# Kernel tuning notes

Hardware: AMD Instinct MI355X
Metric: run time of the kernel (lower is better)

Reference implementation:

```python
import jax, jax.numpy as jnp
import numpy as np

GAMMA = 0.01      # rbf gamma (init kwarg)
C = 10            # n_classes (len(nv))
NV = 500          # support vectors per class (equal segments)
# all (i, j) class pairs with i < j, in the original nested-loop order
PAIRS = np.array([(i, j) for i in range(C) for j in range(i + 1, C)], dtype=np.int32)
I_IDX = jnp.asarray(PAIRS[:, 0])  # [45]
J_IDX = jnp.asarray(PAIRS[:, 1])  # [45]


def setup_inputs() -> dict:
    key = jax.random.key(0)
    k1, k2, k3, k4 = jax.random.split(key, 4)
    x = jax.random.normal(k1, (8192, 256), dtype=jnp.float32)
    sv = jax.random.normal(k2, (5000, 256), dtype=jnp.float32)
    a = jax.random.normal(k3, (C - 1, 5000), dtype=jnp.float32) * 0.1  # dual coefs
    b = jax.random.normal(k4, (45,), dtype=jnp.float32) * 0.1          # intercepts per pair
    return {"x": x, "sv": sv, "a": a, "b": b}


def reference(x, sv, a, b):
    # RBF kernel matrix: k[n, s] = exp(-gamma * ||x_n - sv_s||^2)
    x_norm = jnp.sum(x * x, axis=1)[:, None]            # [N, 1]
    sv_norm = jnp.sum(sv * sv, axis=1)[None, :]         # [1, SV]
    k = jnp.exp(-GAMMA * (x_norm + sv_norm) + 2.0 * GAMMA * (x @ sv.T))  # [N, SV]

    N = x.shape[0]
    kr = k.reshape(N, C, NV)           # per-class SV segments
    ar = a.reshape(C - 1, C, NV)       # dual coef rows, segmented the same way
    # T[n, r, c] = sum_m a[r, segment c, m] * k[n, segment c, m]
    # (fuses every inner Python loop of the original into one contraction)
    T = jnp.einsum('ncm,rcm->nrc', kr, ar)              # [N, C-1, C]

    # decision for pair (i, j): a[i, seg j] . k_seg_j + a[j-1, seg i] . k_seg_i + b
    c = T[:, I_IDX, J_IDX] + T[:, J_IDX - 1, I_IDX] + b[None, :]  # [N, 45]

    # pairwise voting: winner i if c > 0 else j; class id = mode of votes
    votes = jnp.where(c > 0, I_IDX[None, :], J_IDX[None, :])      # [N, 45] int32
    counts = jnp.sum(jax.nn.one_hot(votes, C, dtype=jnp.float32), axis=1)  # [N, C]
    # argmax picks the smallest class index on ties, matching torch.mode
    class_ids = jnp.argmax(counts, axis=1).astype(jnp.int32)
    return (class_ids, class_ids)
```

## Files before the change

kernel.cpp:

```cpp
#include <hip/hip_runtime.h>
#include <hip/hip_fp16.h>
#include <cmath>


#define GAMMA 0.01f
constexpr int N  = 8192;
constexpr int D  = 256;
constexpr int S  = 5000;
constexpr int C  = 10;
constexpr int NV = 500;
constexpr int R  = 9;
constexpr int SPAD = 5120;

typedef _Float16 f16x8 __attribute__((ext_vector_type(8)));
typedef _Float16 f16x4 __attribute__((ext_vector_type(4)));
typedef float    f32x4 __attribute__((ext_vector_type(4)));

__device__ __forceinline__ void gload16(const void* g, void* l) {
    __builtin_amdgcn_global_load_lds(
        (const __attribute__((address_space(1))) void*)g,
        (__attribute__((address_space(3))) void*)l, 16, 0, 0);
}

__global__ __launch_bounds__(256) void prep_kernel(const float* __restrict__ x,
                                                   const float* __restrict__ sv,
                                                   _Float16* __restrict__ xh,
                                                   _Float16* __restrict__ xl,
                                                   _Float16* __restrict__ sh,
                                                   _Float16* __restrict__ sl,
                                                   float* __restrict__ xn,
                                                   float* __restrict__ svn) {
    int gid  = blockIdx.x * blockDim.x + threadIdx.x;
    int wid  = gid >> 6;
    int lane = gid & 63;
    if (wid >= N + S) return;
    bool isx = wid < N;
    int  r   = isx ? wid : wid - N;
    const float* row = isx ? (x + (size_t)r * D) : (sv + (size_t)r * D);
    float4 v = reinterpret_cast<const float4*>(row)[lane];
    float s = v.x * v.x + v.y * v.y + v.z * v.z + v.w * v.w;
#pragma unroll
    for (int off = 32; off > 0; off >>= 1) s += __shfl_xor(s, off, 64);
    float vv[4] = {v.x, v.y, v.z, v.w};
    f16x4 h, l;
#pragma unroll
    for (int k = 0; k < 4; ++k) {
        _Float16 hi = (_Float16)vv[k];
        h[k] = hi;
        l[k] = (_Float16)((vv[k] - (float)hi) * 4096.0f);
    }
    size_t o = (size_t)r * D + lane * 4;
    *(f16x4*)((isx ? xh : sh) + o) = h;
    *(f16x4*)((isx ? xl : sl) + o) = l;
    if (lane == 0) (isx ? xn : svn)[r] = s;
}

__global__ __launch_bounds__(256) void prep_a(const float* __restrict__ a,
                                              const float* __restrict__ svn,
                                              _Float16* __restrict__ ah,
                                              _Float16* __restrict__ al,
                                              float* __restrict__ svnp) {
    int idx = blockIdx.x * 256 + threadIdx.x;
    if (idx >= 16 * SPAD) return;
    int r = idx / SPAD, col = idx - r * SPAD;
    int cls = col >> 9, j = col & 511;
    int s = cls * NV + ((j < NV) ? j : NV - 1);
    float av = (r < R && j < NV) ? a[(size_t)r * S + s] : 0.0f;
    _Float16 h = (_Float16)av;
    ah[idx] = h;
    al[idx] = (_Float16)((av - (float)h) * 4096.0f);
    if (r == 0) svnp[col] = svn[s];
}

__global__ __launch_bounds__(256, 3) void svc_gemm(const _Float16* __restrict__ xh,
                                                   const _Float16* __restrict__ xl,
                                                   const _Float16* __restrict__ sh,
                                                   const _Float16* __restrict__ sl,
                                                   const _Float16* __restrict__ ahp,
                                                   const _Float16* __restrict__ alp,
                                                   const float* __restrict__ xnorm,
                                                   const float* __restrict__ svnp,
                                                   float* __restrict__ T) {
    __shared__ _Float16 SVs[2][2][128 * 32];
    __shared__ _Float16 Xs[2][2][64 * 32];

    const int tid  = threadIdx.x;
    const int n0   = blockIdx.x * 64;
    const int cls  = blockIdx.y;
    const int w    = tid >> 6;
    const int lane = tid & 63;
    const int wm   = w >> 1;
    const int wn   = w & 1;
    const int lx   = lane & 15;
    const int quad = lane >> 4;

    float xnr[2];
#pragma unroll
    for (int nt = 0; nt < 2; ++nt)
        xnr[nt] = xnorm[n0 + wn * 32 + nt * 16 + lx];

    int svoff[4], xoff[2];
#pragma unroll
    for (int mt = 0; mt < 4; ++mt) {
        int row = wm * 64 + mt * 16 + lx;
        svoff[mt] = row * 32 + ((quad - (row >> 1)) & 3) * 8;
    }
#pragma unroll
    for (int nt = 0; nt < 2; ++nt) {
        int row = wn * 32 + nt * 16 + lx;
        xoff[nt] = row * 32 + ((quad - (row >> 1)) & 3) * 8;
    }

    const int arow = tid >> 2, ag = tid & 3;
    const int sg   = (ag + (arow >> 1)) & 3;
    const int segend = cls * NV + NV - 1;
    const int ldsw = w * 512;

    auto stage = [&](int ph, int buf) {
        const int ch = ph >> 3, kb = ph & 7;
        const size_t koff = (size_t)(kb * 32 + sg * 8);
        const size_t goX  = (size_t)(n0 + arow) * D + koff;
        gload16(xh + goX, &Xs[buf][0][ldsw]);
        gload16(xl + goX, &Xs[buf][1][ldsw]);
        const int svbase = cls * NV + ch * 128;
        int svr0 = svbase + arow;      if (svr0 > segend) svr0 = segend;
        int svr1 = svbase + arow + 64; if (svr1 > segend) svr1 = segend;
        const size_t go0 = (size_t)svr0 * D + koff;
        const size_t go1 = (size_t)svr1 * D + koff;
        gload16(sh + go0, &SVs[buf][0][ldsw]);
        gload16(sl + go0, &SVs[buf][1][ldsw]);
        gload16(sh + go1, &SVs[buf][0][2048 + ldsw]);
        gload16(sl + go1, &SVs[buf][1][2048 + ldsw]);
    };

    f32x4 accM[4][2], accC[4][2];
#pragma unroll
    for (int mt = 0; mt < 4; ++mt)
#pragma unroll
        for (int nt = 0; nt < 2; ++nt) {
            accM[mt][nt] = (f32x4){0.f, 0.f, 0.f, 0.f};
            accC[mt][nt] = (f32x4){0.f, 0.f, 0.f, 0.f};
        }
    f32x4 accO[2], accOC[2];
#pragma unroll
    for (int nt = 0; nt < 2; ++nt) {
        accO[nt]  = (f32x4){0.f, 0.f, 0.f, 0.f};
        accOC[nt] = (f32x4){0.f, 0.f, 0.f, 0.f};
    }

    stage(0, 0);
    __syncthreads();

    for (int ph = 0; ph < 32; ++ph) {
        const int buf = ph & 1;
        if (ph < 31) stage(ph + 1, buf ^ 1);

        f16x8 Am[2][4], Bx[2][2];
#pragma unroll
        for (int mt = 0; mt < 4; ++mt) {
            Am[0][mt] = *(const f16x8*)(&SVs[buf][0][svoff[mt]]);
            Am[1][mt] = *(const f16x8*)(&SVs[buf][1][svoff[mt]]);
        }
#pragma unroll
        for (int nt = 0; nt < 2; ++nt) {
            Bx[0][nt] = *(const f16x8*)(&Xs[buf][0][xoff[nt]]);
            Bx[1][nt] = *(const f16x8*)(&Xs[buf][1][xoff[nt]]);
        }
#pragma unroll
        for (int mt = 0; mt < 4; ++mt)
#pragma unroll
            for (int nt = 0; nt < 2; ++nt) {
                accM[mt][nt] = __builtin_amdgcn_mfma_f32_16x16x32_f16(
                    Am[0][mt], Bx[0][nt], accM[mt][nt], 0, 0, 0);
                accC[mt][nt] = __builtin_amdgcn_mfma_f32_16x16x32_f16(
                    Am[0][mt], Bx[1][nt], accC[mt][nt], 0, 0, 0);
                accC[mt][nt] = __builtin_amdgcn_mfma_f32_16x16x32_f16(
                    Am[1][mt], Bx[0][nt], accC[mt][nt], 0, 0, 0);
            }

        __syncthreads();

        if ((ph & 7) == 7) {
            const int ch = ph >> 3;
            const int mbase = cls * 512 + ch * 128 + wm * 64;
#pragma unroll
            for (int mt = 0; mt < 4; ++mt) {
                const size_t ao = (size_t)lx * SPAD + mbase + mt * 16 + quad * 4;
                f16x4 afh = *(const f16x4*)(ahp + ao);
                f16x4 afl = *(const f16x4*)(alp + ao);
                float4 sn4 = *(const float4*)(svnp + mbase + mt * 16 + quad * 4);
#pragma unroll
                for (int nt = 0; nt < 2; ++nt) {
                    f16x4 bh, bl;
#pragma unroll
                    for (int reg = 0; reg < 4; ++reg) {
                        float dot = accM[mt][nt][reg]
                                  + accC[mt][nt][reg] * (1.0f / 4096.0f);
                        float e  = fmaf(2.0f * GAMMA, dot,
                                        -GAMMA * (xnr[nt] + sn4[reg]));
                        float kv = __expf(e);
                        _Float16 h = (_Float16)kv;
                        bh[reg] = h;
                        bl[reg] = (_Float16)((kv - (float)h) * 4096.0f);
                    }
                    accO[nt]  = __builtin_amdgcn_mfma_f32_16x16x16f16(
                        afh, bh, accO[nt], 0, 0, 0);
                    accOC[nt] = __builtin_amdgcn_mfma_f32_16x16x16f16(
                        afh, bl, accOC[nt], 0, 0, 0);
                    accOC[nt] = __builtin_amdgcn_mfma_f32_16x16x16f16(
                        afl, bh, accOC[nt], 0, 0, 0);
                    accM[mt][nt] = (f32x4){0.f, 0.f, 0.f, 0.f};
                    accC[mt][nt] = (f32x4){0.f, 0.f, 0.f, 0.f};
                }
            }
        }
    }

    float* scr = (float*)&SVs[0][0][0];
    if (wm == 0) {
#pragma unroll
        for (int nt = 0; nt < 2; ++nt)
#pragma unroll
            for (int reg = 0; reg < 4; ++reg) {
                int base = ((wn * 2 + nt) * 2) * 256 + (quad * 4 + reg) * 16 + lx;
                scr[base]       = accO[nt][reg];
                scr[base + 256] = accOC[nt][reg];
            }
    }
    __syncthreads();
    if (wm == 1) {
#pragma unroll
        for (int nt = 0; nt < 2; ++nt)
#pragma unroll
            for (int reg = 0; reg < 4; ++reg) {
                int r = quad * 4 + reg;
                if (r < R) {
                    int base = ((wn * 2 + nt) * 2) * 256 + r * 16 + lx;
                    float o  = accO[nt][reg]  + scr[base];
                    float oc = accOC[nt][reg] + scr[base + 256];
                    int n = n0 + wn * 32 + nt * 16 + lx;
                    T[(size_t)n * 90 + r * 10 + cls] = o + oc * (1.0f / 4096.0f);
                }
            }
    }
}

__global__ __launch_bounds__(256) void vote_kernel(const float* __restrict__ T,
                                                   const float* __restrict__ b,
                                                   int* __restrict__ out) {
    int n = blockIdx.x * blockDim.x + threadIdx.x;
    if (n >= N) return;
    const float* Tn = T + (size_t)n * 90;
    float tv[90];
#pragma unroll
    for (int i = 0; i < 90; ++i) tv[i] = Tn[i];
    int counts[C];
#pragma unroll
    for (int k = 0; k < C; ++k) counts[k] = 0;
    int p = 0;
#pragma unroll
    for (int i = 0; i < C; ++i) {
#pragma unroll
        for (int j = i + 1; j < C; ++j) {
            float c = tv[i * 10 + j] + tv[(j - 1) * 10 + i] + b[p];
            if (c > 0.f) counts[i]++; else counts[j]++;
            ++p;
        }
    }
    int best = 0;
#pragma unroll
    for (int k = 1; k < C; ++k)
        if (counts[k] > counts[best]) best = k;
    out[n]     = best;
    out[N + n] = best;
}

extern "C" void kernel_launch(void* const* d_in, const int* in_sizes, int n_in,
                              void* d_out, int out_size, void* d_ws, size_t ws_size,
                              hipStream_t stream) {
    const float* x  = (const float*)d_in[0];
    const float* sv = (const float*)d_in[1];
    const float* a  = (const float*)d_in[2];
    const float* b  = (const float*)d_in[3];
    int* out = (int*)d_out;

    char* wp = (char*)d_ws;
    _Float16* xh = (_Float16*)wp;  wp += (size_t)N * D * 2;
    _Float16* xl = (_Float16*)wp;  wp += (size_t)N * D * 2;
    _Float16* sh = (_Float16*)wp;  wp += (size_t)S * D * 2;
    _Float16* sl = (_Float16*)wp;  wp += (size_t)S * D * 2;
    float* xnorm  = (float*)wp;    wp += (size_t)N * 4;
    float* svnorm = (float*)wp;    wp += (size_t)S * 4;
    _Float16* ahp = (_Float16*)wp; wp += (size_t)16 * SPAD * 2;
    _Float16* alp = (_Float16*)wp; wp += (size_t)16 * SPAD * 2;
    float* svnp   = (float*)wp;    wp += (size_t)SPAD * 4;
    float* T      = (float*)wp;

    {
        int waves = N + S;
        prep_kernel<<<(waves * 64 + 255) / 256, 256, 0, stream>>>(
            x, sv, xh, xl, sh, sl, xnorm, svnorm);
    }
    {
        prep_a<<<(16 * SPAD + 255) / 256, 256, 0, stream>>>(
            a, svnorm, ahp, alp, svnp);
    }
    {
        dim3 grid(N / 64, C);
        svc_gemm<<<grid, 256, 0, stream>>>(xh, xl, sh, sl, ahp, alp,
                                           xnorm, svnp, T);
    }
    {
        vote_kernel<<<N / 256, 256, 0, stream>>>(T, b, out);
    }
}
```

Baseline: 168.1 us.

## Merge prep kernels into one launch and transpose T layout for coalesced voting

Folds the dual-coefficient split kernel into the row prep kernel using extra blocks, and writes padded SV norms directly from the row waves, removing one launch and the intermediate svnorm buffer. T is also stored class-pair-major ([90][N]), so the vote kernel's per-thread loads coalesce across threads. The GEMM epilogue now scatters with stride N instead of writing contiguous rows.

```diff
diff --git a/kernel.cpp b/kernel.cpp
--- a/kernel.cpp
+++ b/kernel.cpp
@@ -12,6 +12,9 @@
 constexpr int R  = 9;
 constexpr int SPAD = 5120;
 
+constexpr int ROW_BLOCKS = (N + S) / 4;
+constexpr int A_BLOCKS   = (16 * SPAD) / 256;
+
 typedef _Float16 f16x8 __attribute__((ext_vector_type(8)));
 typedef _Float16 f16x4 __attribute__((ext_vector_type(4)));
 typedef float    f32x4 __attribute__((ext_vector_type(4)));
@@ -24,16 +27,29 @@
 
 __global__ __launch_bounds__(256) void prep_kernel(const float* __restrict__ x,
                                                    const float* __restrict__ sv,
+                                                   const float* __restrict__ a,
                                                    _Float16* __restrict__ xh,
                                                    _Float16* __restrict__ xl,
                                                    _Float16* __restrict__ sh,
                                                    _Float16* __restrict__ sl,
                                                    float* __restrict__ xn,
-                                                   float* __restrict__ svn) {
+                                                   _Float16* __restrict__ ah,
+                                                   _Float16* __restrict__ al,
+                                                   float* __restrict__ svnp) {
+    if (blockIdx.x >= ROW_BLOCKS) {
+        int idx = (blockIdx.x - ROW_BLOCKS) * 256 + threadIdx.x;
+        int r = idx / SPAD, col = idx - r * SPAD;
+        int cls = col >> 9, j = col & 511;
+        int s = cls * NV + ((j < NV) ? j : NV - 1);
+        float av = (r < R && j < NV) ? a[(size_t)r * S + s] : 0.0f;
+        _Float16 h = (_Float16)av;
+        ah[idx] = h;
+        al[idx] = (_Float16)((av - (float)h) * 4096.0f);
+        return;
+    }
     int gid  = blockIdx.x * blockDim.x + threadIdx.x;
     int wid  = gid >> 6;
     int lane = gid & 63;
-    if (wid >= N + S) return;
     bool isx = wid < N;
     int  r   = isx ? wid : wid - N;
     const float* row = isx ? (x + (size_t)r * D) : (sv + (size_t)r * D);
@@ -52,24 +68,16 @@
     size_t o = (size_t)r * D + lane * 4;
     *(f16x4*)((isx ? xh : sh) + o) = h;
     *(f16x4*)((isx ? xl : sl) + o) = l;
-    if (lane == 0) (isx ? xn : svn)[r] = s;
-}
-
-__global__ __launch_bounds__(256) void prep_a(const float* __restrict__ a,
-                                              const float* __restrict__ svn,
-                                              _Float16* __restrict__ ah,
-                                              _Float16* __restrict__ al,
-                                              float* __restrict__ svnp) {
-    int idx = blockIdx.x * 256 + threadIdx.x;
-    if (idx >= 16 * SPAD) return;
-    int r = idx / SPAD, col = idx - r * SPAD;
-    int cls = col >> 9, j = col & 511;
-    int s = cls * NV + ((j < NV) ? j : NV - 1);
-    float av = (r < R && j < NV) ? a[(size_t)r * S + s] : 0.0f;
-    _Float16 h = (_Float16)av;
-    ah[idx] = h;
-    al[idx] = (_Float16)((av - (float)h) * 4096.0f);
-    if (r == 0) svnp[col] = svn[s];
+    if (lane == 0) {
+        if (isx) {
+            xn[r] = s;
+        } else {
+            int cls = r / NV, j = r - cls * NV;
+            svnp[cls * 512 + j] = s;
+            if (j == NV - 1)
+                for (int p = NV; p < 512; ++p) svnp[cls * 512 + p] = s;
+        }
+    }
 }
 
 __global__ __launch_bounds__(256, 3) void svc_gemm(const _Float16* __restrict__ xh,
@@ -239,7 +247,7 @@
                     float o  = accO[nt][reg]  + scr[base];
                     float oc = accOC[nt][reg] + scr[base + 256];
                     int n = n0 + wn * 32 + nt * 16 + lx;
-                    T[(size_t)n * 90 + r * 10 + cls] = o + oc * (1.0f / 4096.0f);
+                    T[(size_t)(r * 10 + cls) * N + n] = o + oc * (1.0f / 4096.0f);
                 }
             }
     }
@@ -250,10 +258,9 @@
                                                    int* __restrict__ out) {
     int n = blockIdx.x * blockDim.x + threadIdx.x;
     if (n >= N) return;
-    const float* Tn = T + (size_t)n * 90;
     float tv[90];
 #pragma unroll
-    for (int i = 0; i < 90; ++i) tv[i] = Tn[i];
+    for (int i = 0; i < 90; ++i) tv[i] = T[(size_t)i * N + n];
     int counts[C];
 #pragma unroll
     for (int k = 0; k < C; ++k) counts[k] = 0;
@@ -290,20 +297,14 @@
     _Float16* sh = (_Float16*)wp;  wp += (size_t)S * D * 2;
     _Float16* sl = (_Float16*)wp;  wp += (size_t)S * D * 2;
     float* xnorm  = (float*)wp;    wp += (size_t)N * 4;
-    float* svnorm = (float*)wp;    wp += (size_t)S * 4;
     _Float16* ahp = (_Float16*)wp; wp += (size_t)16 * SPAD * 2;
     _Float16* alp = (_Float16*)wp; wp += (size_t)16 * SPAD * 2;
     float* svnp   = (float*)wp;    wp += (size_t)SPAD * 4;
     float* T      = (float*)wp;
 
     {
-        int waves = N + S;
-        prep_kernel<<<(waves * 64 + 255) / 256, 256, 0, stream>>>(
-            x, sv, xh, xl, sh, sl, xnorm, svnorm);
-    }
-    {
-        prep_a<<<(16 * SPAD + 255) / 256, 256, 0, stream>>>(
-            a, svnorm, ahp, alp, svnp);
+        prep_kernel<<<ROW_BLOCKS + A_BLOCKS, 256, 0, stream>>>(
+            x, sv, a, xh, xl, sh, sl, xnorm, ahp, alp, svnp);
     }
     {
         dim3 grid(N / 64, C);
```

Result: no change. 166.4 us (-1.0%).
